# Kernel tuning notes

Hardware: AMD Instinct MI355X
Metric: run time of the kernel (lower is better)

Reference implementation:

```python
import jax, jax.numpy as jnp
import numpy as np

N = 500_000   # active sites
C = 128       # channels (inplanes == planes)
H = W = 2048  # underlying 2D grid
K = 9         # 3x3 kernel offsets
EPS = 1e-4    # scn BatchNormalization default eps


def setup_inputs() -> dict:
    # --- build sparse site set and hash-style neighbor table (the scn "rulebook") ---
    rng = np.random.default_rng(0)
    flat = rng.choice(H * W, size=N, replace=False)
    ys, xs = (flat // W).astype(np.int64), (flat % W).astype(np.int64)
    grid = np.full((H, W), N, dtype=np.int32)  # sentinel N = "inactive"
    grid[ys, xs] = np.arange(N, dtype=np.int32)
    offs = [(dy, dx) for dy in (-1, 0, 1) for dx in (-1, 0, 1)]
    nbr = np.empty((N, K), dtype=np.int32)
    for k, (dy, dx) in enumerate(offs):
        yy, xx = ys + dy, xs + dx
        ok = (yy >= 0) & (yy < H) & (xx >= 0) & (xx < W)
        nbr[:, k] = np.where(ok, grid[np.clip(yy, 0, H - 1), np.clip(xx, 0, W - 1)], N)

    key = jax.random.key(0)
    ks = jax.random.split(key, 7)
    scale = 1.0 / np.sqrt(K * C)  # keep activations O(1)
    return {
        "x": jax.random.normal(ks[0], (N, C), jnp.float32),
        "W1": jax.random.normal(ks[1], (K, C, C), jnp.float32) * scale,
        "W2": jax.random.normal(ks[2], (K, C, C), jnp.float32) * scale,
        "gamma1": 1.0 + 0.1 * jax.random.normal(ks[3], (C,), jnp.float32),
        "beta1": 0.1 * jax.random.normal(ks[4], (C,), jnp.float32),
        "gamma2": 1.0 + 0.1 * jax.random.normal(ks[5], (C,), jnp.float32),
        "beta2": 0.1 * jax.random.normal(ks[6], (C,), jnp.float32),
        "nbr": jnp.asarray(nbr),
    }


def _submconv(x, nbr, Wk):
    # Submanifold 3x3 conv: gather active neighbors per offset, matmul, accumulate.
    # Pad with a zero row so sentinel index N contributes nothing.
    xp = jnp.concatenate([x, jnp.zeros((1, x.shape[1]), x.dtype)], axis=0)  # [N+1, Cin]
    out = jnp.zeros((x.shape[0], Wk.shape[2]), x.dtype)
    for k in range(Wk.shape[0]):  # fixed small loop over 9 kernel offsets
        out = out + xp[nbr[:, k]] @ Wk[k]  # gather [N,Cin] then GEMM -> [N,Cout]
    return out


def _bn(h, gamma, beta):
    # BatchNorm over active sites (training-mode batch statistics, biased var)
    mu = jnp.mean(h, axis=0)
    var = jnp.var(h, axis=0)
    return (h - mu) * (gamma * jax.lax.rsqrt(var + EPS)) + beta


def reference(x, W1, W2, gamma1, beta1, gamma2, beta2, nbr):
    h = _submconv(x, nbr, W1)              # conv1 (3x3 submanifold, C->C)
    h = jax.nn.relu(_bn(h, gamma1, beta1))  # bn1 = BatchNormReLU
    h = _submconv(h, nbr, W2)              # conv2 (3x3 submanifold, C->C)
    h = _bn(h, gamma2, beta2)              # bn2 = BatchNormalization
    return jax.nn.relu(h + x)              # AddTable + ReLU (residual)
```

## Files before the change

### kernel.cpp

```cpp
#include <hip/hip_runtime.h>

#define CH 128
#define TM 128
#define BN_EPS 1e-4f

typedef unsigned short u16;
typedef u16 u16x8 __attribute__((ext_vector_type(8)));
typedef short bf16x8 __attribute__((ext_vector_type(8)));
typedef float f32x4 __attribute__((ext_vector_type(4)));

__device__ __forceinline__ float bf2f(u16 u) {
  union { unsigned int i; float f; } v; v.i = ((unsigned int)u) << 16; return v.f;
}
__device__ __forceinline__ u16 f2bf(float f) {
  union { float f; unsigned int i; } v; v.f = f;
  unsigned int r = v.i + 0x7fffu + ((v.i >> 16) & 1u);
  return (u16)(r >> 16);
}
__device__ __forceinline__ void lds_cp16(const void* g, void* l) {
  __builtin_amdgcn_global_load_lds((const __attribute__((address_space(1))) void*)g,
                                   (__attribute__((address_space(3))) void*)l, 16, 0, 0);
}

__global__ __launch_bounds__(256) void prep_x(const float* __restrict__ x,
                                              u16* __restrict__ xb, int Nr) {
  int g = blockIdx.x * 256 + threadIdx.x;
  int total = (Nr + 1) * 16;
  int stride = gridDim.x * 256;
  for (int idx = g; idx < total; idx += stride) {
    u16x8 o;
    if (idx < Nr * 16) {
      const float* s = x + (size_t)idx * 8;
      f32x4 a = *(const f32x4*)s;
      f32x4 b = *(const f32x4*)(s + 4);
      #pragma unroll
      for (int j = 0; j < 4; ++j) { o[j] = f2bf(a[j]); o[4 + j] = f2bf(b[j]); }
    } else {
      #pragma unroll
      for (int j = 0; j < 8; ++j) o[j] = 0;
    }
    *(u16x8*)(xb + (size_t)idx * 8) = o;
  }
}

__global__ void prep_w(const float* __restrict__ W1, const float* __restrict__ W2,
                       u16* __restrict__ Wt1, u16* __restrict__ Wt2) {
  int b = blockIdx.x;
  const float* src = (b < 9) ? W1 : W2;
  u16* dst = (b < 9) ? Wt1 : Wt2;
  int k = (b < 9) ? b : b - 9;
  src += (size_t)k * CH * CH;
  dst += (size_t)k * CH * CH;
  for (int t = threadIdx.x; t < CH * CH; t += blockDim.x) {
    int co = t & 127, ci = t >> 7;
    float v = src[(size_t)ci * CH + co];
    int sw = co * CH + ((((ci >> 3) ^ (co & 7)) << 3) | (ci & 7));
    dst[sw] = f2bf(v);
  }
}

__global__ __launch_bounds__(256, 2)
void conv_k(const u16* __restrict__ in,
            const u16* __restrict__ Wt,
            const int* __restrict__ nbr,
            u16* __restrict__ outh,
            float* __restrict__ gSum, float* __restrict__ gSq, int Nr) {
  __shared__ __align__(16) u16 Abuf[TM * CH];
  __shared__ __align__(16) u16 Bbuf[CH * CH];
  __shared__ int nbrs[TM * 9];
  __shared__ float smSum[CH], smSq[CH];

  const int tid = threadIdx.x;
  const int lane = tid & 63;
  const int w = tid >> 6;
  const int row0 = blockIdx.x * TM;
  const int l15 = lane & 15, lq = lane >> 4;
  const int wr = w >> 1, wc = w & 1;

  if (tid < CH) { smSum[tid] = 0.f; smSq[tid] = 0.f; }
  for (int i = tid; i < TM * 9; i += 256) {
    int r = i / 9;
    nbrs[i] = (row0 + r < Nr) ? nbr[(size_t)row0 * 9 + i] : Nr;
  }
  __syncthreads();

  f32x4 acc[4][4];
  const f32x4 zero = {0.f, 0.f, 0.f, 0.f};
  #pragma unroll
  for (int i = 0; i < 4; ++i)
    #pragma unroll
    for (int j = 0; j < 4; ++j) acc[i][j] = zero;

  for (int k = 0; k < 9; ++k) {
    const int rb = w * 32;
    #pragma unroll
    for (int it = 0; it < 8; ++it) {
      int r = rb + it * 4 + lq;
      int g = nbrs[r * 9 + k];
      int srcChunk = l15 ^ (r & 7);
      const u16* src = in + (size_t)g * CH + (srcChunk << 3);
      lds_cp16(src, &Abuf[(rb + it * 4) * CH]);
    }
    const u16* wsrc = Wt + (size_t)k * CH * CH + w * 4096;
    #pragma unroll
    for (int it = 0; it < 8; ++it) {
      lds_cp16(wsrc + it * 512 + lane * 8, &Bbuf[w * 4096 + it * 512]);
    }
    __syncthreads();

    #pragma unroll
    for (int kc = 0; kc < 4; ++kc) {
      bf16x8 fa[4], fb[4];
      #pragma unroll
      for (int i = 0; i < 4; ++i) {
        int row = wr * 64 + i * 16 + l15;
        int chunk = (kc * 4 + lq) ^ (row & 7);
        fa[i] = *(const bf16x8*)&Abuf[row * CH + chunk * 8];
      }
      #pragma unroll
      for (int j = 0; j < 4; ++j) {
        int co = wc * 64 + j * 16 + l15;
        int chunk = (kc * 4 + lq) ^ (co & 7);
        fb[j] = *(const bf16x8*)&Bbuf[co * CH + chunk * 8];
      }
      #pragma unroll
      for (int i = 0; i < 4; ++i)
        #pragma unroll
        for (int j = 0; j < 4; ++j)
          acc[i][j] = __builtin_amdgcn_mfma_f32_16x16x32_bf16(fa[i], fb[j], acc[i][j], 0, 0, 0);
    }
    __syncthreads();
  }

  #pragma unroll
  for (int j = 0; j < 4; ++j) {
    float s = 0.f, q = 0.f;
    #pragma unroll
    for (int i = 0; i < 4; ++i)
      #pragma unroll
      for (int t = 0; t < 4; ++t) { float v = acc[i][j][t]; s += v; q += v * v; }
    s += __shfl_xor(s, 16); s += __shfl_xor(s, 32);
    q += __shfl_xor(q, 16); q += __shfl_xor(q, 32);
    if (lane < 16) {
      int col = wc * 64 + j * 16 + l15;
      atomicAdd(&smSum[col], s);
      atomicAdd(&smSq[col], q);
    }
  }

  #pragma unroll
  for (int i = 0; i < 4; ++i)
    #pragma unroll
    for (int j = 0; j < 4; ++j) {
      int col = wc * 64 + j * 16 + l15;
      #pragma unroll
      for (int t = 0; t < 4; ++t) {
        int row = wr * 64 + i * 16 + lq * 4 + t;
        int chunk = (col >> 3) ^ (row & 7);
        Abuf[row * CH + chunk * 8 + (col & 7)] = f2bf(acc[i][j][t]);
      }
    }
  __syncthreads();

  if (tid < CH) {
    atomicAdd(&gSum[tid], smSum[tid]);
    atomicAdd(&gSq[tid], smSq[tid]);
  }
  {
    int r = tid >> 1, half = tid & 1;
    if (row0 + r < Nr) {
      #pragma unroll
      for (int i = 0; i < 8; ++i) {
        int c = half * 8 + i;
        int chunk = c ^ (r & 7);
        u16x8 v = *(const u16x8*)&Abuf[r * CH + chunk * 8];
        *(u16x8*)(outh + (size_t)(row0 + r) * CH + c * 8) = v;
      }
    }
  }
}

__global__ void finalize_stats(const float* __restrict__ sum, const float* __restrict__ sq,
                               const float* __restrict__ gamma, const float* __restrict__ beta,
                               float* __restrict__ scale, float* __restrict__ shift, int Nr) {
  int c = threadIdx.x;
  if (c < CH) {
    float inv = 1.f / (float)Nr;
    float mu = sum[c] * inv;
    float var = sq[c] * inv - mu * mu;
    float rs = rsqrtf(var + BN_EPS);
    float sc = gamma[c] * rs;
    scale[c] = sc;
    shift[c] = beta[c] - mu * sc;
  }
}

__global__ __launch_bounds__(256) void apply_bn(const u16* __restrict__ h,
                                                const float* __restrict__ scale,
                                                const float* __restrict__ shift,
                                                u16* __restrict__ a, int Nr) {
  int g = blockIdx.x * 256 + threadIdx.x;
  int coff = (g & 15) * 8;
  float sc[8], sh[8];
  #pragma unroll
  for (int j = 0; j < 8; ++j) { sc[j] = scale[coff + j]; sh[j] = shift[coff + j]; }
  int total = Nr * 16, stride = gridDim.x * 256;
  for (int idx = g; idx < total; idx += stride) {
    u16x8 v = *(const u16x8*)(h + (size_t)idx * 8);
    u16x8 o;
    #pragma unroll
    for (int j = 0; j < 8; ++j) {
      float f = fmaxf(sc[j] * bf2f(v[j]) + sh[j], 0.f);
      o[j] = f2bf(f);
    }
    *(u16x8*)(a + (size_t)idx * 8) = o;
  }
}

__global__ __launch_bounds__(256) void final_k(const u16* __restrict__ h,
                                               const float* __restrict__ x,
                                               const float* __restrict__ scale,
                                               const float* __restrict__ shift,
                                               float* __restrict__ out, int Nr) {
  int g = blockIdx.x * 256 + threadIdx.x;
  int coff = (g & 15) * 8;
  float sc[8], sh[8];
  #pragma unroll
  for (int j = 0; j < 8; ++j) { sc[j] = scale[coff + j]; sh[j] = shift[coff + j]; }
  int total = Nr * 16, stride = gridDim.x * 256;
  for (int idx = g; idx < total; idx += stride) {
    u16x8 v = *(const u16x8*)(h + (size_t)idx * 8);
    const float* xs = x + (size_t)idx * 8;
    f32x4 xa = *(const f32x4*)xs;
    f32x4 xb = *(const f32x4*)(xs + 4);
    f32x4 oa, ob;
    #pragma unroll
    for (int j = 0; j < 4; ++j) {
      oa[j] = fmaxf(sc[j] * bf2f(v[j]) + sh[j] + xa[j], 0.f);
      ob[j] = fmaxf(sc[4 + j] * bf2f(v[4 + j]) + sh[4 + j] + xb[j], 0.f);
    }
    float* os = out + (size_t)idx * 8;
    *(f32x4*)os = oa;
    *(f32x4*)(os + 4) = ob;
  }
}

extern "C" void kernel_launch(void* const* d_in, const int* in_sizes, int n_in,
                              void* d_out, int out_size, void* d_ws, size_t ws_size,
                              hipStream_t stream) {
  const float* x  = (const float*)d_in[0];
  const float* W1 = (const float*)d_in[1];
  const float* W2 = (const float*)d_in[2];
  const float* g1 = (const float*)d_in[3];
  const float* b1 = (const float*)d_in[4];
  const float* g2 = (const float*)d_in[5];
  const float* b2 = (const float*)d_in[6];
  const int* nbr  = (const int*)d_in[7];
  float* out = (float*)d_out;
  const int Nr = in_sizes[0] / CH;

  char* ws = (char*)d_ws;
  size_t offA = 0;
  size_t szA = (size_t)(Nr + 1) * CH * 2;
  size_t offB = (offA + szA + 255) & ~(size_t)255;
  size_t szB = (size_t)Nr * CH * 2;
  size_t offW1 = (offB + szB + 255) & ~(size_t)255;
  size_t offW2 = offW1 + (size_t)9 * CH * CH * 2;
  size_t offS  = offW2 + (size_t)9 * CH * CH * 2;

  u16* bufA = (u16*)(ws + offA);
  u16* bufB = (u16*)(ws + offB);
  u16* Wt1  = (u16*)(ws + offW1);
  u16* Wt2  = (u16*)(ws + offW2);
  float* stats = (float*)(ws + offS);
  float *sum1 = stats,       *sq1 = stats + 128;
  float *sum2 = stats + 256, *sq2 = stats + 384;
  float *sc1 = stats + 512, *sh1 = stats + 640;
  float *sc2 = stats + 768, *sh2 = stats + 896;

  hipMemsetAsync(stats, 0, 512 * sizeof(float), stream);
  prep_x<<<2048, 256, 0, stream>>>(x, bufA, Nr);
  prep_w<<<18, 256, 0, stream>>>(W1, W2, Wt1, Wt2);

  int nblk = (Nr + TM - 1) / TM;
  conv_k<<<nblk, 256, 0, stream>>>(bufA, Wt1, nbr, bufB, sum1, sq1, Nr);
  finalize_stats<<<1, 128, 0, stream>>>(sum1, sq1, g1, b1, sc1, sh1, Nr);
  apply_bn<<<2048, 256, 0, stream>>>(bufB, sc1, sh1, bufA, Nr);
  conv_k<<<nblk, 256, 0, stream>>>(bufA, Wt2, nbr, bufB, sum2, sq2, Nr);
  finalize_stats<<<1, 128, 0, stream>>>(sum2, sq2, g2, b2, sc2, sh2, Nr);
  final_k<<<2048, 256, 0, stream>>>(bufB, x, sc2, sh2, out, Nr);
}
```

Before: 1.041 ms.

## Gather A operands directly into registers with prefetch, drop A LDS buffer

```diff
diff --git a/kernel.cpp b/kernel.cpp
--- a/kernel.cpp
+++ b/kernel.cpp
@@ -59,13 +59,12 @@
   }
 }
 
-__global__ __launch_bounds__(256, 2)
+__global__ __launch_bounds__(256, 3)
 void conv_k(const u16* __restrict__ in,
             const u16* __restrict__ Wt,
             const int* __restrict__ nbr,
             u16* __restrict__ outh,
             float* __restrict__ gSum, float* __restrict__ gSq, int Nr) {
-  __shared__ __align__(16) u16 Abuf[TM * CH];
   __shared__ __align__(16) u16 Bbuf[CH * CH];
   __shared__ int nbrs[TM * 9];
   __shared__ float smSum[CH], smSq[CH];
@@ -75,7 +74,6 @@
   const int w = tid >> 6;
   const int row0 = blockIdx.x * TM;
   const int l15 = lane & 15, lq = lane >> 4;
-  const int wr = w >> 1, wc = w & 1;
 
   if (tid < CH) { smSum[tid] = 0.f; smSq[tid] = 0.f; }
   for (int i = tid; i < TM * 9; i += 256) {
@@ -84,80 +82,84 @@
   }
   __syncthreads();
 
-  f32x4 acc[4][4];
+  f32x4 acc[2][8];
   const f32x4 zero = {0.f, 0.f, 0.f, 0.f};
   #pragma unroll
-  for (int i = 0; i < 4; ++i)
-    #pragma unroll
-    for (int j = 0; j < 4; ++j) acc[i][j] = zero;
+  for (int i = 0; i < 2; ++i)
+    #pragma unroll
+    for (int j = 0; j < 8; ++j) acc[i][j] = zero;
+
+  bf16x8 faA[2][4], faB[2][4];
+  #pragma unroll
+  for (int i = 0; i < 2; ++i) {
+    int g = nbrs[(w * 32 + i * 16 + l15) * 9 + 0];
+    const u16* p = in + (size_t)g * CH + lq * 8;
+    #pragma unroll
+    for (int c = 0; c < 4; ++c) faA[i][c] = *(const bf16x8*)(p + c * 32);
+  }
 
   for (int k = 0; k < 9; ++k) {
-    const int rb = w * 32;
-    #pragma unroll
-    for (int it = 0; it < 8; ++it) {
-      int r = rb + it * 4 + lq;
-      int g = nbrs[r * 9 + k];
-      int srcChunk = l15 ^ (r & 7);
-      const u16* src = in + (size_t)g * CH + (srcChunk << 3);
-      lds_cp16(src, &Abuf[(rb + it * 4) * CH]);
-    }
     const u16* wsrc = Wt + (size_t)k * CH * CH + w * 4096;
     #pragma unroll
-    for (int it = 0; it < 8; ++it) {
+    for (int it = 0; it < 8; ++it)
       lds_cp16(wsrc + it * 512 + lane * 8, &Bbuf[w * 4096 + it * 512]);
+    const int kk = (k < 8) ? k + 1 : 8;
+    #pragma unroll
+    for (int i = 0; i < 2; ++i) {
+      int g = nbrs[(w * 32 + i * 16 + l15) * 9 + kk];
+      const u16* p = in + (size_t)g * CH + lq * 8;
+      #pragma unroll
+      for (int c = 0; c < 4; ++c) faB[i][c] = *(const bf16x8*)(p + c * 32);
     }
     __syncthreads();
 
     #pragma unroll
     for (int kc = 0; kc < 4; ++kc) {
-      bf16x8 fa[4], fb[4];
-      #pragma unroll
-      for (int i = 0; i < 4; ++i) {
-        int row = wr * 64 + i * 16 + l15;
-        int chunk = (kc * 4 + lq) ^ (row & 7);
-        fa[i] = *(const bf16x8*)&Abuf[row * CH + chunk * 8];
-      }
-      #pragma unroll
-      for (int j = 0; j < 4; ++j) {
-        int co = wc * 64 + j * 16 + l15;
+      bf16x8 fb[8];
+      #pragma unroll
+      for (int j = 0; j < 8; ++j) {
+        int co = j * 16 + l15;
         int chunk = (kc * 4 + lq) ^ (co & 7);
         fb[j] = *(const bf16x8*)&Bbuf[co * CH + chunk * 8];
       }
       #pragma unroll
-      for (int i = 0; i < 4; ++i)
+      for (int i = 0; i < 2; ++i)
         #pragma unroll
-        for (int j = 0; j < 4; ++j)
-          acc[i][j] = __builtin_amdgcn_mfma_f32_16x16x32_bf16(fa[i], fb[j], acc[i][j], 0, 0, 0);
+        for (int j = 0; j < 8; ++j)
+          acc[i][j] = __builtin_amdgcn_mfma_f32_16x16x32_bf16(faA[i][kc], fb[j], acc[i][j], 0, 0, 0);
     }
     __syncthreads();
-  }
-
-  #pragma unroll
-  for (int j = 0; j < 4; ++j) {
+    #pragma unroll
+    for (int i = 0; i < 2; ++i)
+      #pragma unroll
+      for (int c = 0; c < 4; ++c) faA[i][c] = faB[i][c];
+  }
+
+  #pragma unroll
+  for (int j = 0; j < 8; ++j) {
     float s = 0.f, q = 0.f;
     #pragma unroll
-    for (int i = 0; i < 4; ++i)
+    for (int i = 0; i < 2; ++i)
       #pragma unroll
       for (int t = 0; t < 4; ++t) { float v = acc[i][j][t]; s += v; q += v * v; }
     s += __shfl_xor(s, 16); s += __shfl_xor(s, 32);
     q += __shfl_xor(q, 16); q += __shfl_xor(q, 32);
     if (lane < 16) {
-      int col = wc * 64 + j * 16 + l15;
-      atomicAdd(&smSum[col], s);
-      atomicAdd(&smSq[col], q);
-    }
-  }
-
-  #pragma unroll
-  for (int i = 0; i < 4; ++i)
-    #pragma unroll
-    for (int j = 0; j < 4; ++j) {
-      int col = wc * 64 + j * 16 + l15;
+      atomicAdd(&smSum[j * 16 + l15], s);
+      atomicAdd(&smSq[j * 16 + l15], q);
+    }
+  }
+
+  #pragma unroll
+  for (int i = 0; i < 2; ++i)
+    #pragma unroll
+    for (int j = 0; j < 8; ++j) {
+      int col = j * 16 + l15;
       #pragma unroll
       for (int t = 0; t < 4; ++t) {
-        int row = wr * 64 + i * 16 + lq * 4 + t;
+        int row = w * 32 + i * 16 + lq * 4 + t;
         int chunk = (col >> 3) ^ (row & 7);
-        Abuf[row * CH + chunk * 8 + (col & 7)] = f2bf(acc[i][j][t]);
+        Bbuf[row * CH + chunk * 8 + (col & 7)] = f2bf(acc[i][j][t]);
       }
     }
   __syncthreads();
@@ -173,37 +175,35 @@
       for (int i = 0; i < 8; ++i) {
         int c = half * 8 + i;
         int chunk = c ^ (r & 7);
-        u16x8 v = *(const u16x8*)&Abuf[r * CH + chunk * 8];
+        u16x8 v = *(const u16x8*)&Bbuf[r * CH + chunk * 8];
         *(u16x8*)(outh + (size_t)(row0 + r) * CH + c * 8) = v;
       }
     }
   }
 }
 
-__global__ void finalize_stats(const float* __restrict__ sum, const float* __restrict__ sq,
-                               const float* __restrict__ gamma, const float* __restrict__ beta,
-                               float* __restrict__ scale, float* __restrict__ shift, int Nr) {
-  int c = threadIdx.x;
-  if (c < CH) {
+__global__ __launch_bounds__(256) void apply_bn(const u16* __restrict__ h,
+                                                const float* __restrict__ sum,
+                                                const float* __restrict__ sq,
+                                                const float* __restrict__ gamma,
+                                                const float* __restrict__ beta,
+                                                u16* __restrict__ a, int Nr) {
+  __shared__ float sSc[CH], sSh[CH];
+  int tid = threadIdx.x;
+  if (tid < CH) {
     float inv = 1.f / (float)Nr;
-    float mu = sum[c] * inv;
-    float var = sq[c] * inv - mu * mu;
-    float rs = rsqrtf(var + BN_EPS);
-    float sc = gamma[c] * rs;
-    scale[c] = sc;
-    shift[c] = beta[c] - mu * sc;
-  }
-}
-
-__global__ __launch_bounds__(256) void apply_bn(const u16* __restrict__ h,
-                                                const float* __restrict__ scale,
-                                                const float* __restrict__ shift,
-                                                u16* __restrict__ a, int Nr) {
-  int g = blockIdx.x * 256 + threadIdx.x;
-  int coff = (g & 15) * 8;
+    float mu = sum[tid] * inv;
+    float var = sq[tid] * inv - mu * mu;
+    float s = gamma[tid] * rsqrtf(var + BN_EPS);
+    sSc[tid] = s;
+    sSh[tid] = beta[tid] - mu * s;
+  }
+  __syncthreads();
+  int coff = (tid & 15) * 8;
   float sc[8], sh[8];
   #pragma unroll
-  for (int j = 0; j < 8; ++j) { sc[j] = scale[coff + j]; sh[j] = shift[coff + j]; }
+  for (int j = 0; j < 8; ++j) { sc[j] = sSc[coff + j]; sh[j] = sSh[coff + j]; }
+  int g = blockIdx.x * 256 + tid;
   int total = Nr * 16, stride = gridDim.x * 256;
   for (int idx = g; idx < total; idx += stride) {
     u16x8 v = *(const u16x8*)(h + (size_t)idx * 8);
@@ -219,14 +219,27 @@
 
 __global__ __launch_bounds__(256) void final_k(const u16* __restrict__ h,
                                                const float* __restrict__ x,
-                                               const float* __restrict__ scale,
-                                               const float* __restrict__ shift,
+                                               const float* __restrict__ sum,
+                                               const float* __restrict__ sq,
+                                               const float* __restrict__ gamma,
+                                               const float* __restrict__ beta,
                                                float* __restrict__ out, int Nr) {
-  int g = blockIdx.x * 256 + threadIdx.x;
-  int coff = (g & 15) * 8;
+  __shared__ float sSc[CH], sSh[CH];
+  int tid = threadIdx.x;
+  if (tid < CH) {
+    float inv = 1.f / (float)Nr;
+    float mu = sum[tid] * inv;
+    float var = sq[tid] * inv - mu * mu;
+    float s = gamma[tid] * rsqrtf(var + BN_EPS);
+    sSc[tid] = s;
+    sSh[tid] = beta[tid] - mu * s;
+  }
+  __syncthreads();
+  int coff = (tid & 15) * 8;
   float sc[8], sh[8];
   #pragma unroll
-  for (int j = 0; j < 8; ++j) { sc[j] = scale[coff + j]; sh[j] = shift[coff + j]; }
+  for (int j = 0; j < 8; ++j) { sc[j] = sSc[coff + j]; sh[j] = sSh[coff + j]; }
+  int g = blockIdx.x * 256 + tid;
   int total = Nr * 16, stride = gridDim.x * 256;
   for (int idx = g; idx < total; idx += stride) {
     u16x8 v = *(const u16x8*)(h + (size_t)idx * 8);
@@ -275,8 +288,6 @@
   float* stats = (float*)(ws + offS);
   float *sum1 = stats,       *sq1 = stats + 128;
   float *sum2 = stats + 256, *sq2 = stats + 384;
-  float *sc1 = stats + 512, *sh1 = stats + 640;
-  float *sc2 = stats + 768, *sh2 = stats + 896;
 
   hipMemsetAsync(stats, 0, 512 * sizeof(float), stream);
   prep_x<<<2048, 256, 0, stream>>>(x, bufA, Nr);
@@ -284,9 +295,7 @@
 
   int nblk = (Nr + TM - 1) / TM;
   conv_k<<<nblk, 256, 0, stream>>>(bufA, Wt1, nbr, bufB, sum1, sq1, Nr);
-  finalize_stats<<<1, 128, 0, stream>>>(sum1, sq1, g1, b1, sc1, sh1, Nr);
-  apply_bn<<<2048, 256, 0, stream>>>(bufB, sc1, sh1, bufA, Nr);
+  apply_bn<<<2048, 256, 0, stream>>>(bufB, sum1, sq1, g1, b1, bufA, Nr);
   conv_k<<<nblk, 256, 0, stream>>>(bufA, Wt2, nbr, bufB, sum2, sq2, Nr);
-  finalize_stats<<<1, 128, 0, stream>>>(sum2, sq2, g2, b2, sc2, sh2, Nr);
-  final_k<<<2048, 256, 0, stream>>>(bufB, x, sc2, sh2, out, Nr);
-}
+  final_k<<<2048, 256, 0, stream>>>(bufB, x, sum2, sq2, g2, b2, out, Nr);
+}
```

Result: slower. 1.126 ms (+8.1%).
